# Kernel optimization log

Hardware: AMD Instinct MI355X
Metric: run time of the kernel (lower is better)

## Reference

```python
import jax, jax.numpy as jnp
import numpy as np
import math

B, T, D = 2, 2048, 1024
H, HD = 16, 64
E, TOPK, HID = 8, 2, 2048
EPS = 1e-6


def setup_inputs() -> dict:
    key = jax.random.key(0)
    ks = jax.random.split(key, 12)
    s = 0.02
    # RoPE freqs: [T, HD//2, 2] (cos, sin)
    inv = 1.0 / (10000.0 ** (np.arange(0, HD, 2, dtype=np.float32) / HD))
    ang = np.outer(np.arange(T, dtype=np.float32), inv)  # [T, HD//2]
    freqs_cis = jnp.asarray(np.stack([np.cos(ang), np.sin(ang)], axis=-1))
    # causal additive mask [T, T]
    mask = jnp.where(jnp.tril(jnp.ones((T, T), dtype=bool)), 0.0, -jnp.inf).astype(jnp.float32)
    return {
        "x": jax.random.normal(ks[0], (B, T, D), jnp.float32),
        "freqs_cis": freqs_cis,
        "mask": mask,
        "attn_norm_w": jnp.ones((D,), jnp.float32),
        "ffn_norm_w": jnp.ones((D,), jnp.float32),
        "wq": jax.random.normal(ks[1], (D, D), jnp.float32) * s,
        "wk": jax.random.normal(ks[2], (D, D), jnp.float32) * s,
        "wv": jax.random.normal(ks[3], (D, D), jnp.float32) * s,
        "wo": jax.random.normal(ks[4], (D, D), jnp.float32) * s,
        "gate_w": jax.random.normal(ks[5], (D, E), jnp.float32) * s,
        "w1": jax.random.normal(ks[6], (E, D, HID), jnp.float32) * s,
        "w2": jax.random.normal(ks[7], (E, HID, D), jnp.float32) * s,
        "w3": jax.random.normal(ks[8], (E, D, HID), jnp.float32) * s,
    }


def rmsnorm(x, w):
    rms = jax.lax.rsqrt(jnp.mean(x * x, axis=-1, keepdims=True) + EPS)
    return x * rms * w


def rope(q, fc):
    # q: [B, T, H, HD], fc: [T, HD//2, 2]
    qr = q.reshape(*q.shape[:-1], HD // 2, 2)
    cos = fc[None, :, None, :, 0]
    sin = fc[None, :, None, :, 1]
    r0 = qr[..., 0] * cos - qr[..., 1] * sin
    r1 = qr[..., 0] * sin + qr[..., 1] * cos
    return jnp.stack([r0, r1], axis=-1).reshape(q.shape)


def reference(x, freqs_cis, mask, attn_norm_w, ffn_norm_w, wq, wk, wv, wo,
              gate_w, w1, w2, w3):
    # ---- attention sub-block (pre-norm) ----
    h = rmsnorm(x, attn_norm_w)
    q = (h @ wq).reshape(B, T, H, HD)
    k = (h @ wk).reshape(B, T, H, HD)
    v = (h @ wv).reshape(B, T, H, HD)
    q = rope(q, freqs_cis)
    k = rope(k, freqs_cis)
    new_k, new_v = k, v  # kv cache (no prior cache)
    scale = 1.0 / math.sqrt(HD)
    scores = jnp.einsum("bqhd,bkhd->bhqk", q, k) * scale + mask[None, None]
    attn = jax.nn.softmax(scores, axis=-1)
    out = jnp.einsum("bhqk,bkhd->bqhd", attn, v).reshape(B, T, D)
    x = x + out @ wo

    # ---- MoE sub-block (pre-norm) ----
    hf = rmsnorm(x, ffn_norm_w).reshape(-1, D)  # [N, D]
    gate_probs = jax.nn.softmax(hf @ gate_w, axis=-1)  # [N, E]
    topk_vals, topk_idx = jax.lax.top_k(gate_probs, TOPK)
    topk_w = topk_vals / (jnp.sum(topk_vals, axis=-1, keepdims=True) + 1e-8)
    # per-token per-expert combine weight [N, E]
    comb = jnp.sum(topk_w[:, :, None] * jax.nn.one_hot(topk_idx, E), axis=1)
    # dense per-expert SwiGLU (faithful linear combination of expert outputs)
    h1 = jnp.einsum("nd,edh->enh", hf, w1)
    h3 = jnp.einsum("nd,edh->enh", hf, w3)
    y = jnp.einsum("enh,ehd->end", jax.nn.silu(h1) * h3, w2)
    moe_out = jnp.einsum("ne,end->nd", comb, y).reshape(B, T, D)
    x = x + moe_out
    return (x, new_k, new_v)
```

## Files before the change

kernel.cpp:

```cpp
#include <hip/hip_runtime.h>

#define T_SEQ   2048
#define D_MODEL 1024
#define NHEAD   16
#define NEXP    8
#define HID_DIM 2048
#define NTOK    4096
#define MAXBLK  72
#define SLOTS   9216

typedef unsigned short u16;
typedef unsigned int   u32;
typedef __bf16 bf16_t;
typedef bf16_t bf16x8 __attribute__((ext_vector_type(8)));
typedef float  f32x4  __attribute__((ext_vector_type(4)));
typedef float  f32x2  __attribute__((ext_vector_type(2)));
typedef u32    u32x4  __attribute__((ext_vector_type(4)));

typedef __attribute__((address_space(1))) const void* gptr1_t;
typedef __attribute__((address_space(3))) void*       lptr3_t;

__device__ __forceinline__ u16 f2bf_bits(float f) {
  u32 u = __builtin_bit_cast(u32, f);
  u += 0x7FFFu + ((u >> 16) & 1u);
  return (u16)(u >> 16);
}
__device__ __forceinline__ float bf2f(u16 s) {
  return __builtin_bit_cast(float, (u32)s << 16);
}
__device__ __forceinline__ bf16x8 frag_b128(const u16* p) {
  return *reinterpret_cast<const bf16x8*>(p);
}
__device__ __forceinline__ u16 cvt_bf16(float f) {
  return __builtin_bit_cast(u16, (__bf16)f);
}
#define MFMA16(a,b,c) __builtin_amdgcn_mfma_f32_16x16x32_bf16((a),(b),(c),0,0,0)

__device__ __forceinline__ void gload16(const void* g, void* l) {
  __builtin_amdgcn_global_load_lds((gptr1_t)g, (lptr3_t)l, 16, 0, 0);
}

__device__ __forceinline__ void stage128x32(const u16* gbase, size_t ldk, int kt,
                                            u16* lds, int wid, int lane) {
  int rl = lane >> 2, cc = lane & 3;
#pragma unroll
  for (int h = 0; h < 2; ++h) {
    int row = wid*32 + h*16 + rl;
    int chunk = cc ^ ((row >> 1) & 3);
    gload16(gbase + (size_t)row*ldk + kt + chunk*8, lds + (size_t)(wid*32 + h*16)*32);
  }
}
__device__ __forceinline__ bf16x8 fragLDS(const u16* lds, int row, int l4, int l15) {
  int chunk = l4 ^ ((l15 >> 1) & 3);
  return frag_b128(lds + row*32 + chunk*8);
}

template<int SPLIT>
__global__ __launch_bounds__(256) void rmsnorm_kernel(
    const float* __restrict__ x, const float* __restrict__ w,
    u16* __restrict__ hi, u16* __restrict__ lo)
{
  int row = blockIdx.x, tid = threadIdx.x;
  const float* xr = x + (size_t)row * D_MODEL;
  f32x4 v = *reinterpret_cast<const f32x4*>(xr + tid * 4);
  float ss = v[0]*v[0] + v[1]*v[1] + v[2]*v[2] + v[3]*v[3];
#pragma unroll
  for (int off = 32; off >= 1; off >>= 1) ss += __shfl_xor(ss, off);
  __shared__ float part[4];
  if ((tid & 63) == 0) part[tid >> 6] = ss;
  __syncthreads();
  float rms = rsqrtf((part[0]+part[1]+part[2]+part[3]) * (1.0f/D_MODEL) + 1e-6f);
  f32x4 wv = *reinterpret_cast<const f32x4*>(w + tid * 4);
  u32 hw0=0, hw1=0, lw0=0, lw1=0;
#pragma unroll
  for (int j = 0; j < 4; ++j) {
    float f = v[j] * rms * wv[j];
    u16 hb = f2bf_bits(f);
    if (j < 2) hw0 |= (u32)hb << (16*j); else hw1 |= (u32)hb << (16*(j-2));
    if (SPLIT) {
      u16 lb = f2bf_bits(f - bf2f(hb));
      if (j < 2) lw0 |= (u32)lb << (16*j); else lw1 |= (u32)lb << (16*(j-2));
    }
  }
  u32* hp = reinterpret_cast<u32*>(hi + (size_t)row * D_MODEL + tid * 4);
  hp[0] = hw0; hp[1] = hw1;
  if (SPLIT) {
    u32* lp = reinterpret_cast<u32*>(lo + (size_t)row * D_MODEL + tid * 4);
    lp[0] = lw0; lp[1] = lw1;
  }
}

template<int SPLIT>
__global__ __launch_bounds__(256) void transpose_kernel(
    const float* __restrict__ src, u16* __restrict__ dhi, u16* __restrict__ dlo,
    int R, int C)
{
  __shared__ float tile[64][65];
  src += (size_t)blockIdx.z * R * C;
  dhi += (size_t)blockIdx.z * R * C;
  if (SPLIT) dlo += (size_t)blockIdx.z * R * C;
  int r0 = blockIdx.y*64, c0 = blockIdx.x*64;
  int t = threadIdx.x;
  int lr = t>>2, lc4 = (t&3)*16;
#pragma unroll
  for (int i = 0; i < 4; ++i)
    *reinterpret_cast<f32x4*>(&tile[lr][lc4 + i*4]) =
        *reinterpret_cast<const f32x4*>(src + (size_t)(r0+lr)*C + c0 + lc4 + i*4);
  __syncthreads();
#pragma unroll
  for (int h = 0; h < 2; ++h) {
    int oc = h*32 + (t>>3);
    int ok = (t&7)*8;
    union { u16 a[8]; u32x4 v; } hb, lb;
#pragma unroll
    for (int j = 0; j < 8; ++j) {
      float f = tile[ok+j][oc];
      hb.a[j] = f2bf_bits(f);
      if (SPLIT) lb.a[j] = f2bf_bits(f - bf2f(hb.a[j]));
    }
    *reinterpret_cast<u32x4*>(dhi + (size_t)(c0+oc)*R + r0 + ok) = hb.v;
    if (SPLIT)
      *reinterpret_cast<u32x4*>(dlo + (size_t)(c0+oc)*R + r0 + ok) = lb.v;
  }
}

__global__ __launch_bounds__(256) void qkv_gemm_kernel(
    const u16* __restrict__ Ahi, const u16* __restrict__ Alo,
    const u16* __restrict__ Bhi, const u16* __restrict__ Blo,
    const float* __restrict__ freqs,
    u16* __restrict__ qhi, u16* __restrict__ qlo,
    u16* __restrict__ khi, u16* __restrict__ klo,
    u16* __restrict__ vbf, float* __restrict__ kout, float* __restrict__ vout)
{
  const int K = D_MODEL;
  __shared__ __align__(16) u16 AhS[128*32], AlS[128*32], BhS[128*32], BlS[128*32];
  int tid = threadIdx.x, lane = tid & 63, wid = tid >> 6;
  int wm = wid >> 1, wn = wid & 1;
  int l15 = lane & 15, l4 = lane >> 4;
  size_t bm = (size_t)blockIdx.y * 128, bn = (size_t)blockIdx.x * 128;
  const u16* Ah0 = Ahi + bm*K;  const u16* Al0 = Alo + bm*K;
  const u16* Bh0 = Bhi + bn*K;  const u16* Bl0 = Blo + bn*K;
  f32x4 acc[4][4] = {};
  for (int kt = 0; kt < K; kt += 32) {
    __syncthreads();
    stage128x32(Ah0, K, kt, AhS, wid, lane);
    stage128x32(Al0, K, kt, AlS, wid, lane);
    stage128x32(Bh0, K, kt, BhS, wid, lane);
    stage128x32(Bl0, K, kt, BlS, wid, lane);
    __syncthreads();
    bf16x8 ah[4], al[4];
#pragma unroll
    for (int mi = 0; mi < 4; ++mi) {
      int row = wm*64 + mi*16 + l15;
      ah[mi] = fragLDS(AhS, row, l4, l15);
      al[mi] = fragLDS(AlS, row, l4, l15);
    }
#pragma unroll
    for (int ni = 0; ni < 4; ++ni) {
      int row = wn*64 + ni*16 + l15;
      bf16x8 bh = fragLDS(BhS, row, l4, l15);
      bf16x8 bl = fragLDS(BlS, row, l4, l15);
#pragma unroll
      for (int mi = 0; mi < 4; ++mi) {
        acc[mi][ni] = MFMA16(ah[mi], bh, acc[mi][ni]);
        acc[mi][ni] = MFMA16(ah[mi], bl, acc[mi][ni]);
        acc[mi][ni] = MFMA16(al[mi], bh, acc[mi][ni]);
      }
    }
  }
  int mat = (int)(bn >> 10);
  int colbase = (int)(bn & 1023);
#pragma unroll
  for (int mi = 0; mi < 4; ++mi) {
#pragma unroll
    for (int r = 0; r < 4; ++r) {
      int tok = (int)bm + wm*64 + mi*16 + l4*4 + r;
      int t = tok & (T_SEQ - 1);
#pragma unroll
      for (int ni = 0; ni < 4; ++ni) {
        int col = colbase + wn*64 + ni*16 + l15;
        float v = acc[mi][ni][r];
        if (mat == 2) {
          vbf[(size_t)tok*D_MODEL + col] = f2bf_bits(v);
          vout[(size_t)tok*D_MODEL + col] = v;
        } else {
          int d = col & 63, p = d >> 1;
          f32x2 cs = *reinterpret_cast<const f32x2*>(freqs + ((size_t)t*32 + p)*2);
          float partner = __shfl_xor(v, 1);
          float rot = (d & 1) ? (partner*cs[1] + v*cs[0]) : (v*cs[0] - partner*cs[1]);
          u16 hb = f2bf_bits(rot);
          u16 lb = f2bf_bits(rot - bf2f(hb));
          if (mat == 0) {
            qhi[(size_t)tok*D_MODEL + col] = hb;
            qlo[(size_t)tok*D_MODEL + col] = lb;
          } else {
            khi[(size_t)tok*D_MODEL + col] = hb;
            klo[(size_t)tok*D_MODEL + col] = lb;
            kout[(size_t)tok*D_MODEL + col] = rot;
          }
        }
      }
    }
  }
}

__global__ __launch_bounds__(256) void wo_gemm_kernel(
    const u16* __restrict__ A, const u16* __restrict__ Bt,
    const float* __restrict__ resid, float* __restrict__ Cout)
{
  const int K = D_MODEL, N = D_MODEL;
  __shared__ __align__(16) u16 As[128*32], Bs[128*32];
  int tid = threadIdx.x, lane = tid & 63, wid = tid >> 6;
  int wm = wid >> 1, wn = wid & 1;
  int l15 = lane & 15, l4 = lane >> 4;
  size_t bm = (size_t)blockIdx.y * 128, bn = (size_t)blockIdx.x * 128;
  const u16* A0 = A + bm*K;  const u16* B0 = Bt + bn*K;
  f32x4 acc[4][4] = {};
  for (int kt = 0; kt < K; kt += 32) {
    __syncthreads();
    stage128x32(A0, K, kt, As, wid, lane);
    stage128x32(B0, K, kt, Bs, wid, lane);
    __syncthreads();
    bf16x8 a[4];
#pragma unroll
    for (int mi = 0; mi < 4; ++mi)
      a[mi] = fragLDS(As, wm*64 + mi*16 + l15, l4, l15);
#pragma unroll
    for (int ni = 0; ni < 4; ++ni) {
      bf16x8 b = fragLDS(Bs, wn*64 + ni*16 + l15, l4, l15);
#pragma unroll
      for (int mi = 0; mi < 4; ++mi)
        acc[mi][ni] = MFMA16(a[mi], b, acc[mi][ni]);
    }
  }
#pragma unroll
  for (int mi = 0; mi < 4; ++mi)
#pragma unroll
    for (int ni = 0; ni < 4; ++ni)
#pragma unroll
      for (int r = 0; r < 4; ++r) {
        size_t row = bm + wm*64 + mi*16 + l4*4 + r;
        size_t col = bn + wn*64 + ni*16 + l15;
        Cout[row*N + col] = resid[row*N + col] + acc[mi][ni][r];
      }
}

__global__ __launch_bounds__(64) void wg2_kernel(
    const float* __restrict__ wo, const float* __restrict__ ffnw,
    const float* __restrict__ gw, float* __restrict__ wg2)
{
  int d = blockIdx.x, lane = threadIdx.x;
  const float* wr = wo + (size_t)d * D_MODEL;
  float acc[8] = {0,0,0,0,0,0,0,0};
#pragma unroll
  for (int i = 0; i < 4; ++i) {
    int c = lane*4 + i*256;
    f32x4 wv = *reinterpret_cast<const f32x4*>(wr + c);
    f32x4 fv = *reinterpret_cast<const f32x4*>(ffnw + c);
#pragma unroll
    for (int j = 0; j < 4; ++j) {
      float a = wv[j] * fv[j];
      f32x4 g0 = *reinterpret_cast<const f32x4*>(gw + (size_t)(c + j)*NEXP);
      f32x4 g1 = *reinterpret_cast<const f32x4*>(gw + (size_t)(c + j)*NEXP + 4);
      acc[0]+=a*g0[0]; acc[1]+=a*g0[1]; acc[2]+=a*g0[2]; acc[3]+=a*g0[3];
      acc[4]+=a*g1[0]; acc[5]+=a*g1[1]; acc[6]+=a*g1[2]; acc[7]+=a*g1[3];
    }
  }
#pragma unroll
  for (int off = 32; off >= 1; off >>= 1)
#pragma unroll
    for (int e = 0; e < 8; ++e) acc[e] += __shfl_xor(acc[e], off);
  if (lane == 0) {
#pragma unroll
    for (int e = 0; e < 8; ++e) wg2[(size_t)d*NEXP + e] = acc[e];
  }
}

__global__ __launch_bounds__(256) void vg_kernel(
    const float* __restrict__ vf, const float* __restrict__ wg2, float* __restrict__ Vg)
{
  int tok = blockIdx.x * 4 + (threadIdx.x >> 6);
  int lane = threadIdx.x & 63;
  int hh = lane >> 2, part = lane & 3;
  const float* vr = vf + (size_t)tok * D_MODEL + hh*64 + part*16;
  const float* gr = wg2 + (size_t)(hh*64 + part*16) * NEXP;
  float acc[8] = {0,0,0,0,0,0,0,0};
#pragma unroll
  for (int i = 0; i < 4; ++i) {
    f32x4 vv = *reinterpret_cast<const f32x4*>(vr + i*4);
#pragma unroll
    for (int j = 0; j < 4; ++j) {
      float a = vv[j];
      f32x4 g0 = *reinterpret_cast<const f32x4*>(gr + (size_t)(i*4 + j)*NEXP);
      f32x4 g1 = *reinterpret_cast<const f32x4*>(gr + (size_t)(i*4 + j)*NEXP + 4);
      acc[0]+=a*g0[0]; acc[1]+=a*g0[1]; acc[2]+=a*g0[2]; acc[3]+=a*g0[3];
      acc[4]+=a*g1[0]; acc[5]+=a*g1[1]; acc[6]+=a*g1[2]; acc[7]+=a*g1[3];
    }
  }
#pragma unroll
  for (int off = 1; off < 4; off <<= 1)
#pragma unroll
    for (int e = 0; e < 8; ++e) acc[e] += __shfl_xor(acc[e], off);
  if (part == 0) {
#pragma unroll
    for (int e = 0; e < 8; ++e) Vg[((size_t)tok*NHEAD + hh)*NEXP + e] = acc[e];
  }
}

__global__ __launch_bounds__(256) void attn_kernel(
    const u16* __restrict__ Qhi, const u16* __restrict__ Qlo,
    const u16* __restrict__ Khi, const u16* __restrict__ Klo,
    const u16* __restrict__ Vb, const float* __restrict__ Vg,
    u16* __restrict__ Ob, float* __restrict__ raw_ao)
{
  int id = blockIdx.x;
  int bh = id & 31, b = bh >> 4, h = bh & 15;
  int pid = id >> 5;
  int tid = threadIdx.x, lane = tid & 63, wid = tid >> 6;
  int l15 = lane & 15, l4 = lane >> 4;

  __shared__ __align__(16) u16 VT[64][88];
  __shared__ __align__(16) u16 Pl[4][16][72];
  __shared__ float VgS[64][12];

  int vkey = tid >> 2, vd = (tid & 3) * 16;
  int vco = vkey + (vd >> 1);

  for (int ph = 0; ph < 2; ++ph) {
    int qt = ph ? (31 - pid) : pid;
    size_t qoff = ((size_t)(b*T_SEQ + qt*64 + wid*16)) * D_MODEL + h*64;
    bf16x8 qhiF[2], qloF[2];
#pragma unroll
    for (int s = 0; s < 2; ++s) {
      qhiF[s] = frag_b128(Qhi + qoff + (size_t)l15*D_MODEL + s*32 + l4*8);
      qloF[s] = frag_b128(Qlo + qoff + (size_t)l15*D_MODEL + s*32 + l4*8);
    }
    float m_r[4], l_r[4];
    f32x4 racc4[4][2] = {};
    f32x4 oacc[4] = {};
#pragma unroll
    for (int r = 0; r < 4; ++r) { m_r[r] = -1e30f; l_r[r] = 0.f; }

    for (int kt = 0; kt <= qt; ++kt) {
      __syncthreads();
      {
        const u16* vsrc = Vb + ((size_t)(b*T_SEQ + kt*64 + vkey))*D_MODEL + h*64 + vd;
        union { u32x4 u[2]; u16 s[16]; } tv;
        tv.u[0] = *reinterpret_cast<const u32x4*>(vsrc);
        tv.u[1] = *reinterpret_cast<const u32x4*>(vsrc + 8);
#pragma unroll
        for (int j = 0; j < 16; ++j) VT[vd + j][vco] = tv.s[j];
      }
      if (tid < 128) {
        int key = tid >> 1, eh = (tid & 1) * 4;
        const float* gsrc = Vg + ((size_t)(b*T_SEQ + kt*64 + key)*NHEAD + h)*NEXP + eh;
        *reinterpret_cast<f32x4*>(&VgS[key][eh]) = *reinterpret_cast<const f32x4*>(gsrc);
      }
      f32x4 sacc[4] = {};
      const u16* kbaseH = Khi + ((size_t)(b*T_SEQ + kt*64))*D_MODEL + h*64;
      const u16* kbaseL = Klo + ((size_t)(b*T_SEQ + kt*64))*D_MODEL + h*64;
      __builtin_amdgcn_s_setprio(1);
#pragma unroll
      for (int n = 0; n < 4; ++n) {
#pragma unroll
        for (int s = 0; s < 2; ++s) {
          size_t koff = (size_t)(n*16 + l15)*D_MODEL + s*32 + l4*8;
          bf16x8 khiF = frag_b128(kbaseH + koff);
          bf16x8 kloF = frag_b128(kbaseL + koff);
          sacc[n] = MFMA16(qhiF[s], khiF, sacc[n]);
          sacc[n] = MFMA16(qhiF[s], kloF, sacc[n]);
          sacc[n] = MFMA16(qloF[s], khiF, sacc[n]);
        }
      }
      __builtin_amdgcn_s_setprio(0);
#pragma unroll
      for (int n = 0; n < 4; ++n)
#pragma unroll
        for (int r = 0; r < 4; ++r)
          sacc[n][r] *= 0.125f;
      if (kt == qt) {
        int q0 = qt*64 + wid*16 + l4*4;
        int k00 = kt*64 + l15;
#pragma unroll
        for (int n = 0; n < 4; ++n)
#pragma unroll
          for (int r = 0; r < 4; ++r)
            if (k00 + n*16 > q0 + r) sacc[n][r] = -1e30f;
      }
      float rm[4];
#pragma unroll
      for (int r = 0; r < 4; ++r) {
        float v = fmaxf(fmaxf(sacc[0][r], sacc[1][r]), fmaxf(sacc[2][r], sacc[3][r]));
#pragma unroll
        for (int off = 1; off < 16; off <<= 1) v = fmaxf(v, __shfl_xor(v, off));
        rm[r] = v;
      }
      int needp = (rm[0] > m_r[0]+8.f) | (rm[1] > m_r[1]+8.f) |
                  (rm[2] > m_r[2]+8.f) | (rm[3] > m_r[3]+8.f);
      if (__any(needp)) {
#pragma unroll
        for (int r = 0; r < 4; ++r) {
          float mn = fmaxf(m_r[r], rm[r]);
          float corr = __expf(m_r[r] - mn);
          m_r[r] = mn;
          l_r[r] *= corr;
          racc4[r][0] *= corr; racc4[r][1] *= corr;
#pragma unroll
          for (int n = 0; n < 4; ++n) oacc[n][r] *= corr;
        }
      }
#pragma unroll
      for (int r = 0; r < 4; ++r) {
        float rs = 0.f;
#pragma unroll
        for (int n = 0; n < 4; ++n) {
          float pp = __expf(sacc[n][r] - m_r[r]);
          sacc[n][r] = pp;
          rs += pp;
        }
#pragma unroll
        for (int off = 1; off < 16; off <<= 1) rs += __shfl_xor(rs, off);
        l_r[r] += rs;
      }
#pragma unroll
      for (int n = 0; n < 4; ++n)
#pragma unroll
        for (int r = 0; r < 4; ++r)
          Pl[wid][l4*4 + r][n*16 + l15] = cvt_bf16(sacc[n][r]);
      __syncthreads();
#pragma unroll
      for (int n = 0; n < 4; ++n) {
        f32x4 g0 = *reinterpret_cast<const f32x4*>(&VgS[n*16 + l15][0]);
        f32x4 g1 = *reinterpret_cast<const f32x4*>(&VgS[n*16 + l15][4]);
#pragma unroll
        for (int r = 0; r < 4; ++r) {
          float pp = sacc[n][r];
          racc4[r][0] += g0 * pp;
          racc4[r][1] += g1 * pp;
        }
      }
      __builtin_amdgcn_s_setprio(1);
#pragma unroll
      for (int s = 0; s < 2; ++s) {
        bf16x8 pa = frag_b128(&Pl[wid][l15][s*32 + l4*8]);
#pragma unroll
        for (int n = 0; n < 4; ++n) {
          bf16x8 vb8 = frag_b128(&VT[n*16 + l15][s*32 + l4*8 + 8*n]);
          oacc[n] = MFMA16(pa, vb8, oacc[n]);
        }
      }
      __builtin_amdgcn_s_setprio(0);
    }
    float inv[4];
#pragma unroll
    for (int r = 0; r < 4; ++r) inv[r] = 1.0f / l_r[r];
    size_t obase = ((size_t)(b*T_SEQ + qt*64 + wid*16))*D_MODEL + h*64;
#pragma unroll
    for (int n = 0; n < 4; ++n)
#pragma unroll
      for (int r = 0; r < 4; ++r)
        Ob[obase + (size_t)(l4*4 + r)*D_MODEL + n*16 + l15] = cvt_bf16(oacc[n][r]*inv[r]);
    float rv[4][8];
#pragma unroll
    for (int r = 0; r < 4; ++r)
#pragma unroll
      for (int e = 0; e < 8; ++e)
        rv[r][e] = (e < 4) ? racc4[r][0][e] : racc4[r][1][e-4];
#pragma unroll
    for (int off = 1; off < 16; off <<= 1)
#pragma unroll
      for (int r = 0; r < 4; ++r)
#pragma unroll
        for (int e = 0; e < 8; ++e)
          rv[r][e] += __shfl_xor(rv[r][e], off);
    if (l15 == 0) {
#pragma unroll
      for (int r = 0; r < 4; ++r) {
        size_t tokg = (size_t)(b*T_SEQ) + qt*64 + wid*16 + l4*4 + r;
#pragma unroll
        for (int e = 0; e < 8; ++e)
          raw_ao[(tokg*NHEAD + h)*NEXP + e] = rv[r][e]*inv[r];
      }
    }
  }
}

__global__ void zero_counts_kernel(int* counts) {
  if (threadIdx.x < NEXP) counts[threadIdx.x] = 0;
}

__global__ __launch_bounds__(256) void gate2_kernel(
    const float* __restrict__ x, const float* __restrict__ x2,
    const float* __restrict__ ffnw, const float* __restrict__ gw,
    const float* __restrict__ raw_ao,
    int* __restrict__ gidx, float* __restrict__ gwt, int* __restrict__ counts)
{
  int tok = blockIdx.x * 4 + (threadIdx.x >> 6);
  int lane = threadIdx.x & 63;
  const float* xr = x + (size_t)tok * D_MODEL;
  const float* x2r = x2 + (size_t)tok * D_MODEL;
  float ss = 0.f;
  float lg[8] = {0,0,0,0,0,0,0,0};
#pragma unroll
  for (int i = 0; i < 4; ++i) {
    int d = lane*4 + i*256;
    f32x4 xv = *reinterpret_cast<const f32x4*>(xr + d);
    f32x4 x2v = *reinterpret_cast<const f32x4*>(x2r + d);
    f32x4 wv = *reinterpret_cast<const f32x4*>(ffnw + d);
    ss += x2v[0]*x2v[0] + x2v[1]*x2v[1] + x2v[2]*x2v[2] + x2v[3]*x2v[3];
#pragma unroll
    for (int j = 0; j < 4; ++j) {
      float a = xv[j]*wv[j];
      f32x4 g0 = *reinterpret_cast<const f32x4*>(gw + (size_t)(d + j)*NEXP);
      f32x4 g1 = *reinterpret_cast<const f32x4*>(gw + (size_t)(d + j)*NEXP + 4);
      lg[0]+=a*g0[0]; lg[1]+=a*g0[1]; lg[2]+=a*g0[2]; lg[3]+=a*g0[3];
      lg[4]+=a*g1[0]; lg[5]+=a*g1[1]; lg[6]+=a*g1[2]; lg[7]+=a*g1[3];
    }
  }
#pragma unroll
  for (int off = 1; off < 64; off <<= 1) {
    ss += __shfl_xor(ss, off);
#pragma unroll
    for (int e = 0; e < 8; ++e) lg[e] += __shfl_xor(lg[e], off);
  }
  float ah[8] = {0,0,0,0,0,0,0,0};
  if (lane < 16) {
    const float* ar = raw_ao + ((size_t)tok*NHEAD + lane)*NEXP;
#pragma unroll
    for (int e = 0; e < 8; ++e) ah[e] = ar[e];
  }
#pragma unroll
  for (int off = 1; off < 16; off <<= 1)
#pragma unroll
    for (int e = 0; e < 8; ++e) ah[e] += __shfl_xor(ah[e], off);
  if (lane == 0) {
    float rms = rsqrtf(ss*(1.0f/D_MODEL) + 1e-6f);
    float lo_[8], pp[8];
    float mx = -1e30f;
#pragma unroll
    for (int e = 0; e < 8; ++e) { lo_[e] = (lg[e] + ah[e]) * rms; mx = fmaxf(mx, lo_[e]); }
    float sum = 0.f;
#pragma unroll
    for (int e = 0; e < 8; ++e) { pp[e] = __expf(lo_[e] - mx); sum += pp[e]; }
    float isum = 1.0f/sum;
#pragma unroll
    for (int e = 0; e < 8; ++e) pp[e] *= isum;
    int i0 = 0;
    for (int e = 1; e < 8; ++e) if (pp[e] > pp[i0]) i0 = e;
    int i1 = (i0 == 0) ? 1 : 0;
    for (int e = 0; e < 8; ++e) if (e != i0 && pp[e] > pp[i1]) i1 = e;
    float v0 = pp[i0], v1 = pp[i1];
    float wnorm = 1.0f/(v0 + v1 + 1e-8f);
    gidx[2*tok] = i0; gidx[2*tok+1] = i1;
    gwt[2*tok] = v0*wnorm; gwt[2*tok+1] = v1*wnorm;
    atomicAdd(&counts[i0], 1); atomicAdd(&counts[i1], 1);
  }
}

__global__ __launch_bounds__(256) void scan_kernel(
    const int* __restrict__ counts, int* __restrict__ base, int* __restrict__ fill,
    int* __restrict__ blk_expert, int* __restrict__ perm_token)
{
  if (threadIdx.x == 0) {
    int b = 0, blk = 0;
    for (int e = 0; e < NEXP; ++e) {
      base[e] = b;
      fill[e] = 0;
      int nb = (counts[e] + 127) >> 7;
      for (int i = 0; i < nb; ++i) blk_expert[blk++] = e;
      b += nb << 7;
    }
    for (; blk < MAXBLK; ++blk) blk_expert[blk] = -1;
  }
  for (int i = threadIdx.x; i < SLOTS; i += 256) perm_token[i] = -1;
}

__global__ __launch_bounds__(256) void scatter_kernel(
    const int* __restrict__ gidx, const int* __restrict__ base, int* __restrict__ fill,
    int* __restrict__ perm_token, int* __restrict__ tok_slot)
{
  int t = blockIdx.x * 256 + threadIdx.x;
  if (t >= NTOK) return;
#pragma unroll
  for (int r = 0; r < 2; ++r) {
    int e = gidx[2*t + r];
    int pos = base[e] + atomicAdd(&fill[e], 1);
    perm_token[pos] = t;
    tok_slot[2*t + r] = pos;
  }
}

__global__ __launch_bounds__(256) void moe_gemm1_kernel(
    const u16* __restrict__ Ah, const u16* __restrict__ W1t, const u16* __restrict__ W3t,
    const int* __restrict__ perm_token, const int* __restrict__ blk_expert,
    u16* __restrict__ tbuf)
{
  int mb = blockIdx.y;
  int e = blk_expert[mb];
  if (e < 0) return;
  const int K = D_MODEL;
  __shared__ __align__(16) u16 As[128*32], B1s[128*32], B3s[128*32];
  int tid = threadIdx.x, lane = tid & 63, wid = tid >> 6;
  int wm = wid >> 1, wn = wid & 1;
  int l15 = lane & 15, l4 = lane >> 4;
  size_t bn = (size_t)blockIdx.x * 128;
  const u16* w1e = W1t + (size_t)e * HID_DIM * D_MODEL + bn*K;
  const u16* w3e = W3t + (size_t)e * HID_DIM * D_MODEL + bn*K;
  int rl = lane >> 2, cc = lane & 3;
  int tokA[2];
#pragma unroll
  for (int h = 0; h < 2; ++h) {
    int row = wid*32 + h*16 + rl;
    int t = perm_token[mb*128 + row];
    tokA[h] = t < 0 ? 0 : t;
  }
  f32x4 acc1[4][4] = {}, acc3[4][4] = {};
  for (int kt = 0; kt < K; kt += 32) {
    __syncthreads();
#pragma unroll
    for (int h = 0; h < 2; ++h) {
      int row = wid*32 + h*16 + rl;
      int chunk = cc ^ ((row >> 1) & 3);
      gload16(Ah + (size_t)tokA[h]*K + kt + chunk*8, As + (size_t)(wid*32 + h*16)*32);
    }
    stage128x32(w1e, K, kt, B1s, wid, lane);
    stage128x32(w3e, K, kt, B3s, wid, lane);
    __syncthreads();
    bf16x8 a[4];
#pragma unroll
    for (int mi = 0; mi < 4; ++mi)
      a[mi] = fragLDS(As, wm*64 + mi*16 + l15, l4, l15);
#pragma unroll
    for (int ni = 0; ni < 4; ++ni) {
      int row = wn*64 + ni*16 + l15;
      bf16x8 b1 = fragLDS(B1s, row, l4, l15);
      bf16x8 b3 = fragLDS(B3s, row, l4, l15);
#pragma unroll
      for (int mi = 0; mi < 4; ++mi) {
        acc1[mi][ni] = MFMA16(a[mi], b1, acc1[mi][ni]);
        acc3[mi][ni] = MFMA16(a[mi], b3, acc3[mi][ni]);
      }
    }
  }
#pragma unroll
  for (int mi = 0; mi < 4; ++mi)
#pragma unroll
    for (int ni = 0; ni < 4; ++ni)
#pragma unroll
      for (int r = 0; r < 4; ++r) {
        size_t slot = (size_t)mb*128 + wm*64 + mi*16 + l4*4 + r;
        size_t col = bn + wn*64 + ni*16 + l15;
        float h1 = acc1[mi][ni][r], h3 = acc3[mi][ni][r];
        float sil = h1 / (1.0f + __expf(-h1));
        tbuf[slot*HID_DIM + col] = f2bf_bits(sil * h3);
      }
}

__global__ __launch_bounds__(256) void moe_gemm2_kernel(
    const u16* __restrict__ tbuf, const u16* __restrict__ W2t,
    const int* __restrict__ blk_expert, u16* __restrict__ ybuf)
{
  int mb = blockIdx.y;
  int e = blk_expert[mb];
  if (e < 0) return;
  const int K = HID_DIM, N = D_MODEL;
  __shared__ __align__(16) u16 As[128*32], Bs[128*32];
  int tid = threadIdx.x, lane = tid & 63, wid = tid >> 6;
  int wm = wid >> 1, wn = wid & 1;
  int l15 = lane & 15, l4 = lane >> 4;
  size_t bm = (size_t)mb * 128, bn = (size_t)blockIdx.x * 128;
  const u16* A0 = tbuf + bm*K;
  const u16* B0 = W2t + (size_t)e * D_MODEL * HID_DIM + bn*K;
  f32x4 acc[4][4] = {};
  for (int kt = 0; kt < K; kt += 32) {
    __syncthreads();
    stage128x32(A0, K, kt, As, wid, lane);
    stage128x32(B0, K, kt, Bs, wid, lane);
    __syncthreads();
    bf16x8 a[4];
#pragma unroll
    for (int mi = 0; mi < 4; ++mi)
      a[mi] = fragLDS(As, wm*64 + mi*16 + l15, l4, l15);
#pragma unroll
    for (int ni = 0; ni < 4; ++ni) {
      bf16x8 b = fragLDS(Bs, wn*64 + ni*16 + l15, l4, l15);
#pragma unroll
      for (int mi = 0; mi < 4; ++mi)
        acc[mi][ni] = MFMA16(a[mi], b, acc[mi][ni]);
    }
  }
#pragma unroll
  for (int mi = 0; mi < 4; ++mi)
#pragma unroll
    for (int ni = 0; ni < 4; ++ni)
#pragma unroll
      for (int r = 0; r < 4; ++r) {
        size_t slot = bm + wm*64 + mi*16 + l4*4 + r;
        size_t col = bn + wn*64 + ni*16 + l15;
        ybuf[slot*N + col] = f2bf_bits(acc[mi][ni][r]);
      }
}

__global__ __launch_bounds__(256) void combine_kernel(
    const float* __restrict__ x2, const u16* __restrict__ ybuf,
    const int* __restrict__ tok_slot, const float* __restrict__ gwt,
    float* __restrict__ xout)
{
  int t = blockIdx.x;
  int c = threadIdx.x * 4;
  int s0 = tok_slot[2*t], s1 = tok_slot[2*t+1];
  float w0 = gwt[2*t], w1 = gwt[2*t+1];
  f32x4 xv = *reinterpret_cast<const f32x4*>(x2 + (size_t)t * D_MODEL + c);
  const u16* y0 = ybuf + (size_t)s0 * D_MODEL + c;
  const u16* y1 = ybuf + (size_t)s1 * D_MODEL + c;
  f32x4 o;
#pragma unroll
  for (int j = 0; j < 4; ++j)
    o[j] = xv[j] + w0 * bf2f(y0[j]) + w1 * bf2f(y1[j]);
  *reinterpret_cast<f32x4*>(xout + (size_t)t * D_MODEL + c) = o;
}

extern "C" void kernel_launch(void* const* d_in, const int* in_sizes, int n_in,
                              void* d_out, int out_size, void* d_ws, size_t ws_size,
                              hipStream_t stream)
{
  (void)in_sizes; (void)n_in; (void)out_size; (void)ws_size;
  const float* x     = (const float*)d_in[0];
  const float* freqs = (const float*)d_in[1];
  const float* attnw = (const float*)d_in[3];
  const float* ffnw  = (const float*)d_in[4];
  const float* wq    = (const float*)d_in[5];
  const float* wk    = (const float*)d_in[6];
  const float* wv    = (const float*)d_in[7];
  const float* wo    = (const float*)d_in[8];
  const float* gw    = (const float*)d_in[9];
  const float* w1    = (const float*)d_in[10];
  const float* w2    = (const float*)d_in[11];
  const float* w3    = (const float*)d_in[12];
  float* xout = (float*)d_out;
  float* kout = xout + (size_t)NTOK * D_MODEL;
  float* vout = kout + (size_t)NTOK * D_MODEL;

  const size_t PLANE = (size_t)NTOK * D_MODEL * 2;
  const size_t QKVT  = (size_t)3 * D_MODEL * D_MODEL * 2;
  const size_t TBUFB = (size_t)SLOTS * HID_DIM * 2;
  const size_t WEXP  = (size_t)NEXP * D_MODEL * HID_DIM * 2;
  char* base = (char*)d_ws;
  u16* hhi      = (u16*)(base);
  u16* hlo      = (u16*)(base + PLANE);
  u16* wqkvT_hi = (u16*)(base + 2*PLANE);
  u16* wqkvT_lo = (u16*)(base + 2*PLANE + QKVT);
  u16* woT      = (u16*)(base + 2*PLANE);
  u16* tbuf     = (u16*)(base);
  char* Qb = base + TBUFB;
  u16* qhi = (u16*)(Qb);
  u16* qlo = (u16*)(Qb + PLANE);
  u16* khi = (u16*)(Qb + 2*PLANE);
  u16* klo = (u16*)(Qb + 3*PLANE);
  u16* vbf = (u16*)(Qb + 4*PLANE);
  u16* w1T  = (u16*)(Qb);
  u16* ybuf = (u16*)(Qb);
  char* Sb = Qb + 5*PLANE;
  u16* aobf = (u16*)(Sb);
  u16* w3T  = (u16*)(Sb);
  u16* w2T  = (u16*)(Sb);
  char* Tb = Sb + WEXP;
  u16* hf = (u16*)(Tb);
  float* x2 = (float*)(Tb + PLANE);
  char* p = Tb + PLANE + (size_t)NTOK * D_MODEL * 4;
  float* wg2    = (float*)p;  p += 32768;
  float* Vg     = (float*)p;  p += (size_t)NTOK*NHEAD*NEXP*4;
  float* raw_ao = (float*)p;  p += (size_t)NTOK*NHEAD*NEXP*4;
  int*   gidx   = (int*)p;    p += 32768;
  float* gwt    = (float*)p;  p += 32768;
  int*   tok_slot = (int*)p;  p += 32768;
  int*   perm   = (int*)p;    p += SLOTS*4;
  int*   counts = (int*)p;
  int*   base_  = counts + 8;
  int*   fill_  = counts + 16;
  int*   blk_e  = counts + 24;

  dim3 blk(256);
  rmsnorm_kernel<1><<<NTOK, blk, 0, stream>>>(x, attnw, hhi, hlo);
  wg2_kernel<<<D_MODEL, 64, 0, stream>>>(wo, ffnw, gw, wg2);
  zero_counts_kernel<<<1, 64, 0, stream>>>(counts);
  dim3 tg(16, 16);
  transpose_kernel<1><<<tg, blk, 0, stream>>>(wq, wqkvT_hi,                   wqkvT_lo,                   D_MODEL, D_MODEL);
  transpose_kernel<1><<<tg, blk, 0, stream>>>(wk, wqkvT_hi + (size_t)D_MODEL*D_MODEL,   wqkvT_lo + (size_t)D_MODEL*D_MODEL,   D_MODEL, D_MODEL);
  transpose_kernel<1><<<tg, blk, 0, stream>>>(wv, wqkvT_hi + (size_t)2*D_MODEL*D_MODEL, wqkvT_lo + (size_t)2*D_MODEL*D_MODEL, D_MODEL, D_MODEL);
  dim3 gqkv(24, 32);
  qkv_gemm_kernel<<<gqkv, blk, 0, stream>>>(hhi, hlo, wqkvT_hi, wqkvT_lo, freqs,
                                            qhi, qlo, khi, klo, vbf, kout, vout);
  transpose_kernel<0><<<tg, blk, 0, stream>>>(wo, woT, nullptr, D_MODEL, D_MODEL);
  vg_kernel<<<NTOK/4, blk, 0, stream>>>(vout, wg2, Vg);
  attn_kernel<<<dim3(512), blk, 0, stream>>>(qhi, qlo, khi, klo, vbf, Vg, aobf, raw_ao);
  dim3 tw13(HID_DIM/64, D_MODEL/64, NEXP);
  transpose_kernel<0><<<tw13, blk, 0, stream>>>(w1, w1T, nullptr, D_MODEL, HID_DIM);
  dim3 g88(D_MODEL/128, NTOK/128);
  wo_gemm_kernel<<<g88, blk, 0, stream>>>(aobf, woT, x, x2);
  transpose_kernel<0><<<tw13, blk, 0, stream>>>(w3, w3T, nullptr, D_MODEL, HID_DIM);
  rmsnorm_kernel<0><<<NTOK, blk, 0, stream>>>(x2, ffnw, hf, nullptr);
  gate2_kernel<<<NTOK/4, blk, 0, stream>>>(x, x2, ffnw, gw, raw_ao, gidx, gwt, counts);
  scan_kernel<<<1, blk, 0, stream>>>(counts, base_, fill_, blk_e, perm);
  scatter_kernel<<<NTOK/256, blk, 0, stream>>>(gidx, base_, fill_, perm, tok_slot);
  dim3 g1(HID_DIM/128, MAXBLK);
  moe_gemm1_kernel<<<g1, blk, 0, stream>>>(hf, w1T, w3T, perm, blk_e, tbuf);
  dim3 tw2(D_MODEL/64, HID_DIM/64, NEXP);
  transpose_kernel<0><<<tw2, blk, 0, stream>>>(w2, w2T, nullptr, HID_DIM, D_MODEL);
  dim3 g2(D_MODEL/128, MAXBLK);
  moe_gemm2_kernel<<<g2, blk, 0, stream>>>(tbuf, w2T, blk_e, ybuf);
  combine_kernel<<<NTOK, blk, 0, stream>>>(x2, ybuf, tok_slot, gwt, xout);
}
```

Before: 859.1 us.

## Deepen MoE GEMM K-tiles, pack epilogue stores, shrink Wo tile, fuse QKV transposes

The MoE GEMM1 and GEMM2 kernels now stage 64-wide K tiles with an XOR swizzle, which halves the number of barrier/load rounds at the cost of more LDS per block. Epilogues in the QKV, Wo and MoE GEMMs exchange values between lane pairs so each even lane writes a packed pair, reducing the number of narrow global stores. The Wo GEMM switches to a 128x64 tile to launch more blocks, with a launch bound of 4 blocks per SM. The three QKV weight transposes are merged into one launch, and SiLU uses a fast reciprocal instead of a division.

```diff
diff --git a/kernel.cpp b/kernel.cpp
--- a/kernel.cpp
+++ b/kernel.cpp
@@ -50,9 +50,31 @@
     gload16(gbase + (size_t)row*ldk + kt + chunk*8, lds + (size_t)(wid*32 + h*16)*32);
   }
 }
+__device__ __forceinline__ void stage64x32(const u16* gbase, size_t ldk, int kt,
+                                           u16* lds, int wid, int lane) {
+  int rl = lane >> 2, cc = lane & 3;
+  int row = wid*16 + rl;
+  int chunk = cc ^ ((row >> 1) & 3);
+  gload16(gbase + (size_t)row*ldk + kt + chunk*8, lds + (size_t)(wid*16)*32);
+}
 __device__ __forceinline__ bf16x8 fragLDS(const u16* lds, int row, int l4, int l15) {
   int chunk = l4 ^ ((l15 >> 1) & 3);
   return frag_b128(lds + row*32 + chunk*8);
+}
+
+__device__ __forceinline__ void stage128x64(const u16* gbase, size_t ldk, int kt,
+                                            u16* lds, int wid, int lane) {
+  int rl = lane >> 3, cc = lane & 7;
+#pragma unroll
+  for (int g = 0; g < 4; ++g) {
+    int row = wid*32 + g*8 + rl;
+    int chunk = cc ^ (row & 7);
+    gload16(gbase + (size_t)row*ldk + kt + chunk*8, lds + (size_t)(wid*32 + g*8)*64);
+  }
+}
+__device__ __forceinline__ bf16x8 fragLDS64(const u16* lds, int row, int s, int l4, int l15) {
+  int chunk = (s*4 + l4) ^ (l15 & 7);
+  return frag_b128(lds + row*64 + chunk*8);
 }
 
 template<int SPLIT>
@@ -121,6 +143,39 @@
     *reinterpret_cast<u32x4*>(dhi + (size_t)(c0+oc)*R + r0 + ok) = hb.v;
     if (SPLIT)
       *reinterpret_cast<u32x4*>(dlo + (size_t)(c0+oc)*R + r0 + ok) = lb.v;
+  }
+}
+
+__global__ __launch_bounds__(256) void transpose_qkv_kernel(
+    const float* __restrict__ wq, const float* __restrict__ wk, const float* __restrict__ wv,
+    u16* __restrict__ dhi, u16* __restrict__ dlo)
+{
+  __shared__ float tile[64][65];
+  int z = blockIdx.z;
+  const float* src = (z == 0) ? wq : ((z == 1) ? wk : wv);
+  dhi += (size_t)z * D_MODEL * D_MODEL;
+  dlo += (size_t)z * D_MODEL * D_MODEL;
+  int r0 = blockIdx.y*64, c0 = blockIdx.x*64;
+  int t = threadIdx.x;
+  int lr = t>>2, lc4 = (t&3)*16;
+#pragma unroll
+  for (int i = 0; i < 4; ++i)
+    *reinterpret_cast<f32x4*>(&tile[lr][lc4 + i*4]) =
+        *reinterpret_cast<const f32x4*>(src + (size_t)(r0+lr)*D_MODEL + c0 + lc4 + i*4);
+  __syncthreads();
+#pragma unroll
+  for (int h = 0; h < 2; ++h) {
+    int oc = h*32 + (t>>3);
+    int ok = (t&7)*8;
+    union { u16 a[8]; u32x4 v; } hb, lb;
+#pragma unroll
+    for (int j = 0; j < 8; ++j) {
+      float f = tile[ok+j][oc];
+      hb.a[j] = f2bf_bits(f);
+      lb.a[j] = f2bf_bits(f - bf2f(hb.a[j]));
+    }
+    *reinterpret_cast<u32x4*>(dhi + (size_t)(c0+oc)*D_MODEL + r0 + ok) = hb.v;
+    *reinterpret_cast<u32x4*>(dlo + (size_t)(c0+oc)*D_MODEL + r0 + ok) = lb.v;
   }
 }
 
@@ -170,6 +225,7 @@
   }
   int mat = (int)(bn >> 10);
   int colbase = (int)(bn & 1023);
+  int evenl = !(lane & 1);
 #pragma unroll
   for (int mi = 0; mi < 4; ++mi) {
 #pragma unroll
@@ -181,22 +237,32 @@
         int col = colbase + wn*64 + ni*16 + l15;
         float v = acc[mi][ni][r];
         if (mat == 2) {
-          vbf[(size_t)tok*D_MODEL + col] = f2bf_bits(v);
-          vout[(size_t)tok*D_MODEL + col] = v;
+          float vp = __shfl_xor(v, 1);
+          if (evenl) {
+            u32 pk = (u32)cvt_bf16(v) | ((u32)cvt_bf16(vp) << 16);
+            *reinterpret_cast<u32*>(vbf + (size_t)tok*D_MODEL + col) = pk;
+            f32x2 fv; fv[0] = v; fv[1] = vp;
+            *reinterpret_cast<f32x2*>(vout + (size_t)tok*D_MODEL + col) = fv;
+          }
         } else {
           int d = col & 63, p = d >> 1;
           f32x2 cs = *reinterpret_cast<const f32x2*>(freqs + ((size_t)t*32 + p)*2);
           float partner = __shfl_xor(v, 1);
           float rot = (d & 1) ? (partner*cs[1] + v*cs[0]) : (v*cs[0] - partner*cs[1]);
-          u16 hb = f2bf_bits(rot);
-          u16 lb = f2bf_bits(rot - bf2f(hb));
-          if (mat == 0) {
-            qhi[(size_t)tok*D_MODEL + col] = hb;
-            qlo[(size_t)tok*D_MODEL + col] = lb;
-          } else {
-            khi[(size_t)tok*D_MODEL + col] = hb;
-            klo[(size_t)tok*D_MODEL + col] = lb;
-            kout[(size_t)tok*D_MODEL + col] = rot;
+          float rotp = __shfl_xor(rot, 1);
+          if (evenl) {
+            u16 h0 = cvt_bf16(rot), h1 = cvt_bf16(rotp);
+            u32 hp = (u32)h0 | ((u32)h1 << 16);
+            u32 lp = (u32)cvt_bf16(rot - bf2f(h0)) | ((u32)cvt_bf16(rotp - bf2f(h1)) << 16);
+            if (mat == 0) {
+              *reinterpret_cast<u32*>(qhi + (size_t)tok*D_MODEL + col) = hp;
+              *reinterpret_cast<u32*>(qlo + (size_t)tok*D_MODEL + col) = lp;
+            } else {
+              *reinterpret_cast<u32*>(khi + (size_t)tok*D_MODEL + col) = hp;
+              *reinterpret_cast<u32*>(klo + (size_t)tok*D_MODEL + col) = lp;
+              f32x2 fv; fv[0] = rot; fv[1] = rotp;
+              *reinterpret_cast<f32x2*>(kout + (size_t)tok*D_MODEL + col) = fv;
+            }
           }
         }
       }
@@ -204,44 +270,51 @@
   }
 }
 
-__global__ __launch_bounds__(256) void wo_gemm_kernel(
+__global__ __launch_bounds__(256, 4) void wo_gemm_kernel(
     const u16* __restrict__ A, const u16* __restrict__ Bt,
     const float* __restrict__ resid, float* __restrict__ Cout)
 {
   const int K = D_MODEL, N = D_MODEL;
-  __shared__ __align__(16) u16 As[128*32], Bs[128*32];
+  __shared__ __align__(16) u16 As[128*32], Bs[64*32];
   int tid = threadIdx.x, lane = tid & 63, wid = tid >> 6;
   int wm = wid >> 1, wn = wid & 1;
   int l15 = lane & 15, l4 = lane >> 4;
-  size_t bm = (size_t)blockIdx.y * 128, bn = (size_t)blockIdx.x * 128;
+  size_t bm = (size_t)blockIdx.y * 128, bn = (size_t)blockIdx.x * 64;
   const u16* A0 = A + bm*K;  const u16* B0 = Bt + bn*K;
-  f32x4 acc[4][4] = {};
+  f32x4 acc[4][2] = {};
   for (int kt = 0; kt < K; kt += 32) {
     __syncthreads();
     stage128x32(A0, K, kt, As, wid, lane);
-    stage128x32(B0, K, kt, Bs, wid, lane);
+    stage64x32(B0, K, kt, Bs, wid, lane);
     __syncthreads();
     bf16x8 a[4];
 #pragma unroll
     for (int mi = 0; mi < 4; ++mi)
       a[mi] = fragLDS(As, wm*64 + mi*16 + l15, l4, l15);
 #pragma unroll
-    for (int ni = 0; ni < 4; ++ni) {
-      bf16x8 b = fragLDS(Bs, wn*64 + ni*16 + l15, l4, l15);
+    for (int ni = 0; ni < 2; ++ni) {
+      bf16x8 b = fragLDS(Bs, wn*32 + ni*16 + l15, l4, l15);
 #pragma unroll
       for (int mi = 0; mi < 4; ++mi)
         acc[mi][ni] = MFMA16(a[mi], b, acc[mi][ni]);
     }
   }
+  int evenl = !(lane & 1);
 #pragma unroll
   for (int mi = 0; mi < 4; ++mi)
 #pragma unroll
-    for (int ni = 0; ni < 4; ++ni)
+    for (int ni = 0; ni < 2; ++ni)
 #pragma unroll
       for (int r = 0; r < 4; ++r) {
-        size_t row = bm + wm*64 + mi*16 + l4*4 + r;
-        size_t col = bn + wn*64 + ni*16 + l15;
-        Cout[row*N + col] = resid[row*N + col] + acc[mi][ni][r];
+        float v = acc[mi][ni][r];
+        float vp = __shfl_xor(v, 1);
+        if (evenl) {
+          size_t row = bm + wm*64 + mi*16 + l4*4 + r;
+          size_t col = bn + wn*32 + ni*16 + l15;
+          f32x2 rv = *reinterpret_cast<const f32x2*>(resid + row*N + col);
+          f32x2 ov; ov[0] = rv[0] + v; ov[1] = rv[1] + vp;
+          *reinterpret_cast<f32x2*>(Cout + row*N + col) = ov;
+        }
       }
 }
 
@@ -599,49 +672,53 @@
   int e = blk_expert[mb];
   if (e < 0) return;
   const int K = D_MODEL;
-  __shared__ __align__(16) u16 As[128*32], B1s[128*32], B3s[128*32];
+  __shared__ __align__(16) u16 As[128*64], B1s[128*64], B3s[128*64];
   int tid = threadIdx.x, lane = tid & 63, wid = tid >> 6;
   int wm = wid >> 1, wn = wid & 1;
   int l15 = lane & 15, l4 = lane >> 4;
   size_t bn = (size_t)blockIdx.x * 128;
   const u16* w1e = W1t + (size_t)e * HID_DIM * D_MODEL + bn*K;
   const u16* w3e = W3t + (size_t)e * HID_DIM * D_MODEL + bn*K;
-  int rl = lane >> 2, cc = lane & 3;
-  int tokA[2];
-#pragma unroll
-  for (int h = 0; h < 2; ++h) {
-    int row = wid*32 + h*16 + rl;
+  int rl = lane >> 3, cc = lane & 7;
+  int tokA[4];
+#pragma unroll
+  for (int g = 0; g < 4; ++g) {
+    int row = wid*32 + g*8 + rl;
     int t = perm_token[mb*128 + row];
-    tokA[h] = t < 0 ? 0 : t;
+    tokA[g] = t < 0 ? 0 : t;
   }
   f32x4 acc1[4][4] = {}, acc3[4][4] = {};
-  for (int kt = 0; kt < K; kt += 32) {
+  for (int kt = 0; kt < K; kt += 64) {
     __syncthreads();
 #pragma unroll
-    for (int h = 0; h < 2; ++h) {
-      int row = wid*32 + h*16 + rl;
-      int chunk = cc ^ ((row >> 1) & 3);
-      gload16(Ah + (size_t)tokA[h]*K + kt + chunk*8, As + (size_t)(wid*32 + h*16)*32);
-    }
-    stage128x32(w1e, K, kt, B1s, wid, lane);
-    stage128x32(w3e, K, kt, B3s, wid, lane);
+    for (int g = 0; g < 4; ++g) {
+      int row = wid*32 + g*8 + rl;
+      int chunk = cc ^ (row & 7);
+      gload16(Ah + (size_t)tokA[g]*K + kt + chunk*8, As + (size_t)(wid*32 + g*8)*64);
+    }
+    stage128x64(w1e, K, kt, B1s, wid, lane);
+    stage128x64(w3e, K, kt, B3s, wid, lane);
     __syncthreads();
-    bf16x8 a[4];
-#pragma unroll
-    for (int mi = 0; mi < 4; ++mi)
-      a[mi] = fragLDS(As, wm*64 + mi*16 + l15, l4, l15);
-#pragma unroll
-    for (int ni = 0; ni < 4; ++ni) {
-      int row = wn*64 + ni*16 + l15;
-      bf16x8 b1 = fragLDS(B1s, row, l4, l15);
-      bf16x8 b3 = fragLDS(B3s, row, l4, l15);
-#pragma unroll
-      for (int mi = 0; mi < 4; ++mi) {
-        acc1[mi][ni] = MFMA16(a[mi], b1, acc1[mi][ni]);
-        acc3[mi][ni] = MFMA16(a[mi], b3, acc3[mi][ni]);
-      }
-    }
-  }
+#pragma unroll
+    for (int s = 0; s < 2; ++s) {
+      bf16x8 a[4];
+#pragma unroll
+      for (int mi = 0; mi < 4; ++mi)
+        a[mi] = fragLDS64(As, wm*64 + mi*16 + l15, s, l4, l15);
+#pragma unroll
+      for (int ni = 0; ni < 4; ++ni) {
+        int row = wn*64 + ni*16 + l15;
+        bf16x8 b1 = fragLDS64(B1s, row, s, l4, l15);
+        bf16x8 b3 = fragLDS64(B3s, row, s, l4, l15);
+#pragma unroll
+        for (int mi = 0; mi < 4; ++mi) {
+          acc1[mi][ni] = MFMA16(a[mi], b1, acc1[mi][ni]);
+          acc3[mi][ni] = MFMA16(a[mi], b3, acc3[mi][ni]);
+        }
+      }
+    }
+  }
+  int evenl = !(lane & 1);
 #pragma unroll
   for (int mi = 0; mi < 4; ++mi)
 #pragma unroll
@@ -651,8 +728,12 @@
         size_t slot = (size_t)mb*128 + wm*64 + mi*16 + l4*4 + r;
         size_t col = bn + wn*64 + ni*16 + l15;
         float h1 = acc1[mi][ni][r], h3 = acc3[mi][ni][r];
-        float sil = h1 / (1.0f + __expf(-h1));
-        tbuf[slot*HID_DIM + col] = f2bf_bits(sil * h3);
+        float t = h1 * __builtin_amdgcn_rcpf(1.0f + __expf(-h1)) * h3;
+        float tp = __shfl_xor(t, 1);
+        if (evenl) {
+          u32 pk = (u32)cvt_bf16(t) | ((u32)cvt_bf16(tp) << 16);
+          *reinterpret_cast<u32*>(tbuf + slot*HID_DIM + col) = pk;
+        }
       }
 }
 
@@ -664,7 +745,7 @@
   int e = blk_expert[mb];
   if (e < 0) return;
   const int K = HID_DIM, N = D_MODEL;
-  __shared__ __align__(16) u16 As[128*32], Bs[128*32];
+  __shared__ __align__(16) u16 As[128*64], Bs[128*64];
   int tid = threadIdx.x, lane = tid & 63, wid = tid >> 6;
   int wm = wid >> 1, wn = wid & 1;
   int l15 = lane & 15, l4 = lane >> 4;
@@ -672,32 +753,41 @@
   const u16* A0 = tbuf + bm*K;
   const u16* B0 = W2t + (size_t)e * D_MODEL * HID_DIM + bn*K;
   f32x4 acc[4][4] = {};
-  for (int kt = 0; kt < K; kt += 32) {
+  for (int kt = 0; kt < K; kt += 64) {
     __syncthreads();
-    stage128x32(A0, K, kt, As, wid, lane);
-    stage128x32(B0, K, kt, Bs, wid, lane);
+    stage128x64(A0, K, kt, As, wid, lane);
+    stage128x64(B0, K, kt, Bs, wid, lane);
     __syncthreads();
-    bf16x8 a[4];
-#pragma unroll
-    for (int mi = 0; mi < 4; ++mi)
-      a[mi] = fragLDS(As, wm*64 + mi*16 + l15, l4, l15);
-#pragma unroll
-    for (int ni = 0; ni < 4; ++ni) {
-      bf16x8 b = fragLDS(Bs, wn*64 + ni*16 + l15, l4, l15);
+#pragma unroll
+    for (int s = 0; s < 2; ++s) {
+      bf16x8 a[4];
 #pragma unroll
       for (int mi = 0; mi < 4; ++mi)
-        acc[mi][ni] = MFMA16(a[mi], b, acc[mi][ni]);
-    }
-  }
+        a[mi] = fragLDS64(As, wm*64 + mi*16 + l15, s, l4, l15);
+#pragma unroll
+      for (int ni = 0; ni < 4; ++ni) {
+        bf16x8 b = fragLDS64(Bs, wn*64 + ni*16 + l15, s, l4, l15);
+#pragma unroll
+        for (int mi = 0; mi < 4; ++mi)
+          acc[mi][ni] = MFMA16(a[mi], b, acc[mi][ni]);
+      }
+    }
+  }
+  int evenl = !(lane & 1);
 #pragma unroll
   for (int mi = 0; mi < 4; ++mi)
 #pragma unroll
     for (int ni = 0; ni < 4; ++ni)
 #pragma unroll
       for (int r = 0; r < 4; ++r) {
-        size_t slot = bm + wm*64 + mi*16 + l4*4 + r;
-        size_t col = bn + wn*64 + ni*16 + l15;
-        ybuf[slot*N + col] = f2bf_bits(acc[mi][ni][r]);
+        float v = acc[mi][ni][r];
+        float vp = __shfl_xor(v, 1);
+        if (evenl) {
+          size_t slot = bm + wm*64 + mi*16 + l4*4 + r;
+          size_t col = bn + wn*64 + ni*16 + l15;
+          u32 pk = (u32)cvt_bf16(v) | ((u32)cvt_bf16(vp) << 16);
+          *reinterpret_cast<u32*>(ybuf + slot*N + col) = pk;
+        }
       }
 }
 
@@ -784,19 +874,18 @@
   rmsnorm_kernel<1><<<NTOK, blk, 0, stream>>>(x, attnw, hhi, hlo);
   wg2_kernel<<<D_MODEL, 64, 0, stream>>>(wo, ffnw, gw, wg2);
   zero_counts_kernel<<<1, 64, 0, stream>>>(counts);
-  dim3 tg(16, 16);
-  transpose_kernel<1><<<tg, blk, 0, stream>>>(wq, wqkvT_hi,                   wqkvT_lo,                   D_MODEL, D_MODEL);
-  transpose_kernel<1><<<tg, blk, 0, stream>>>(wk, wqkvT_hi + (size_t)D_MODEL*D_MODEL,   wqkvT_lo + (size_t)D_MODEL*D_MODEL,   D_MODEL, D_MODEL);
-  transpose_kernel<1><<<tg, blk, 0, stream>>>(wv, wqkvT_hi + (size_t)2*D_MODEL*D_MODEL, wqkvT_lo + (size_t)2*D_MODEL*D_MODEL, D_MODEL, D_MODEL);
+  dim3 tg3(16, 16, 3);
+  transpose_qkv_kernel<<<tg3, blk, 0, stream>>>(wq, wk, wv, wqkvT_hi, wqkvT_lo);
   dim3 gqkv(24, 32);
   qkv_gemm_kernel<<<gqkv, blk, 0, stream>>>(hhi, hlo, wqkvT_hi, wqkvT_lo, freqs,
                                             qhi, qlo, khi, klo, vbf, kout, vout);
+  dim3 tg(16, 16);
   transpose_kernel<0><<<tg, blk, 0, stream>>>(wo, woT, nullptr, D_MODEL, D_MODEL);
   vg_kernel<<<NTOK/4, blk, 0, stream>>>(vout, wg2, Vg);
   attn_kernel<<<dim3(512), blk, 0, stream>>>(qhi, qlo, khi, klo, vbf, Vg, aobf, raw_ao);
   dim3 tw13(HID_DIM/64, D_MODEL/64, NEXP);
   transpose_kernel<0><<<tw13, blk, 0, stream>>>(w1, w1T, nullptr, D_MODEL, HID_DIM);
-  dim3 g88(D_MODEL/128, NTOK/128);
+  dim3 g88(D_MODEL/64, NTOK/128);
   wo_gemm_kernel<<<g88, blk, 0, stream>>>(aobf, woT, x, x2);
   transpose_kernel<0><<<tw13, blk, 0, stream>>>(w3, w3T, nullptr, D_MODEL, HID_DIM);
   rmsnorm_kernel<0><<<NTOK, blk, 0, stream>>>(x2, ffnw, hf, nullptr);
```

Result: slower. 894.9 us (+4.2%).
